# Kernel tuning notes

Hardware: AMD Instinct MI355X
Metric: run time of the kernel (lower is better)

## Reference

```python
import jax, jax.numpy as jnp
import numpy as np

N, C, T, V = 16, 64, 634, 26
K, TK = 3, 9          # spatial / temporal kernel sizes
NCLS, NAE = 60, 4     # num_classes, num_att_edge
D = C * V             # transformer d_model = 1664
NH = 4
HD = D // NH
DFF = 128
EPS = 1e-5


def _bn(x, g, b, m, v, axis=1):
    # inference-mode BatchNorm with running stats
    sh = [1] * x.ndim
    sh[axis] = -1
    return (x - m.reshape(sh)) * jax.lax.rsqrt(v.reshape(sh) + EPS) * g.reshape(sh) + b.reshape(sh)


def _ln(x, g, b):
    mu = x.mean(-1, keepdims=True)
    var = jnp.mean((x - mu) ** 2, -1, keepdims=True)
    return (x - mu) * jax.lax.rsqrt(var + EPS) * g + b


def setup_inputs() -> dict:
    ks = iter(jax.random.split(jax.random.key(0), 64))
    nrm = lambda sh, s=0.05: jax.random.normal(next(ks), sh, jnp.float32) * s
    pos = lambda sh: jax.random.uniform(next(ks), sh, jnp.float32) * 0.5 + 0.5
    return dict(
        x=jax.random.normal(next(ks), (N, C, T, V), jnp.float32),
        A=jax.random.uniform(next(ks), (K, V, V), jnp.float32) / V,
        sgc_w=nrm((3, K * C, C)), sgc_b=nrm((3, K * C)),
        M=jnp.ones((3, K, V, V), jnp.float32),
        bnA_g=pos((3, C)), bnA_b=nrm((3, C)), bnA_m=nrm((3, C)), bnA_v=pos((3, C)),
        tconv_w=nrm((3, C, C, TK)), tconv_b=nrm((3, C)),
        bnB_g=pos((3, C)), bnB_b=nrm((3, C)), bnB_m=nrm((3, C)), bnB_v=pos((3, C)),
        fc_w=nrm((NCLS, C)), fc_b=nrm((NCLS,)),
        attbn_g=pos((C,)), attbn_b=nrm((C,)), attbn_m=nrm((C,)), attbn_v=pos((C,)),
        tbn_g=pos((T,)), tbn_b=nrm((T,)), tbn_m=nrm((T,)), tbn_v=pos((T,)),
        attn_w=nrm((4, D, D), 0.02), attn_b=nrm((4, D)),
        ln1_g=pos((D,)), ln1_b=nrm((D,)),
        ff1_w=nrm((D, DFF), 0.02), ff1_b=nrm((DFF,)),
        ff2_w=nrm((DFF, D), 0.02), ff2_b=nrm((D,)),
        ln2_g=pos((D,)), ln2_b=nrm((D,)),
        attconv_w=nrm((NCLS, C)),
        nodeconv_w=nrm((1, NCLS)),
        nodebn_g=pos((1,)), nodebn_b=nrm((1,)), nodebn_m=nrm((1,)), nodebn_v=pos((1,)),
        edgeconv_w=nrm((NAE * V, NCLS)),
        edgebn_g=pos((NAE * V,)), edgebn_b=nrm((NAE * V,)), edgebn_m=nrm((NAE * V,)), edgebn_v=pos((NAE * V,)),
    )


def reference(x, A, sgc_w, sgc_b, M, bnA_g, bnA_b, bnA_m, bnA_v, tconv_w, tconv_b,
              bnB_g, bnB_b, bnB_m, bnB_v, fc_w, fc_b, attbn_g, attbn_b, attbn_m, attbn_v,
              tbn_g, tbn_b, tbn_m, tbn_v, attn_w, attn_b, ln1_g, ln1_b, ff1_w, ff1_b,
              ff2_w, ff2_b, ln2_g, ln2_b, attconv_w, nodeconv_w, nodebn_g, nodebn_b,
              nodebn_m, nodebn_v, edgeconv_w, edgebn_g, edgebn_b, edgebn_m, edgebn_v):
    h = x
    for i in range(3):  # three STGC blocks (eval-mode BN, dropout off)
        y = jnp.einsum('nctv,oc->notv', h, sgc_w[i]) + sgc_b[i][None, :, None, None]
        y = y.reshape(N, K, C, T, V)
        y = jnp.einsum('nkctv,kvw->nctw', y, A * M[i])          # spatial graph conv
        y = jax.nn.relu(_bn(y, bnA_g[i], bnA_b[i], bnA_m[i], bnA_v[i]))
        y = jax.lax.conv_general_dilated(
            y, tconv_w[i][:, :, :, None], (1, 1),
            ((TK // 2, TK // 2), (0, 0)),
            dimension_numbers=('NCHW', 'OIHW', 'NCHW')) + tconv_b[i][None, :, None, None]
        h = jax.nn.relu(_bn(y, bnB_g[i], bnB_b[i], bnB_m[i], bnB_v[i]))
    # classification head: global avg pool + 1x1 conv (== linear)
    output = h.mean((2, 3)) @ fc_w.T + fc_b                     # [N, NCLS]
    x_att = _bn(h, attbn_g, attbn_b, attbn_m, attbn_v)
    # transformer branch: computed in the original but its result is never
    # used by the returned tensors (att_mat is only printed)
    xt = h.transpose(0, 2, 1, 3).reshape(N, T, D)
    xt = _bn(xt, tbn_g, tbn_b, tbn_m, tbn_v, axis=1)            # BatchNorm1d over T channels
    q, k, v = (((xt @ attn_w[j] + attn_b[j]).reshape(N, T, NH, HD).transpose(0, 2, 1, 3)) for j in range(3))
    attn = jax.nn.softmax(jnp.einsum('nhqd,nhkd->nhqk', q, k) / HD ** 0.5, axis=-1)
    ao = jnp.einsum('nhqk,nhkd->nhqd', attn, v).transpose(0, 2, 1, 3).reshape(N, T, D)
    ao = ao @ attn_w[3] + attn_b[3]
    xb = _ln(xt + ao, ln1_g, ln1_b)
    ff = jax.nn.relu(xb @ ff1_w + ff1_b) @ ff2_w + ff2_b
    _dead = _ln(xb + ff, ln2_g, ln2_b)                          # dead: not returned
    # node attention
    x_att = jnp.einsum('nctv,oc->notv', x_att, attconv_w)       # [N, NCLS, T, V]
    x_node = jnp.einsum('nctv,oc->notv', x_att, nodeconv_w)     # [N, 1, T, V]
    x_node = _bn(x_node, nodebn_g, nodebn_b, nodebn_m, nodebn_v)
    att_node = jax.nn.sigmoid(x_node)                           # interpolate to (T,V) is identity here
    # edge attention
    x_edge = x_att.mean(2, keepdims=True)                       # avg pool over T: [N, NCLS, 1, V]
    x_edge = jnp.einsum('nctv,oc->notv', x_edge, edgeconv_w)    # [N, NAE*V, 1, V]
    x_edge = _bn(x_edge, edgebn_g, edgebn_b, edgebn_m, edgebn_v)
    att_edge = jax.nn.relu(jnp.tanh(x_edge.reshape(N, NAE, V, V)))
    return (output, att_node, att_edge)
```

## Files before the change

### kernel.cpp

```cpp
#include <hip/hip_runtime.h>
#include <hip/hip_bf16.h>
#include <math.h>

#define NN 16
#define CC 64
#define TT_ 634
#define VV 26
#define TV 16484
#define KK 3
#define OO 192
#define TKK 9
#define NCLS 60
#define NAE 4
#define EPS 1e-5f

typedef __attribute__((ext_vector_type(8))) short short8;
typedef __attribute__((ext_vector_type(4))) float f32x4;

static __device__ __forceinline__ float bf2f(unsigned int u) {
  union { unsigned int i; float f; } v; v.i = u << 16; return v.f;
}
static __device__ __forceinline__ unsigned int f2bf(float x) {
  union { float f; unsigned int i; } v; v.f = x;
  unsigned int r = v.i + 0x7fffu + ((v.i >> 16) & 1u);
  return r >> 16;
}

#define W1_ELEMS (3 * OO * CC)
#define W2_ELEMS (3 * CC * 576)
#define AM_ELEMS (3 * KK * 1024)

__global__ __launch_bounds__(256) void k_prep_all(
    const float* __restrict__ sgc_w, const float* __restrict__ tconv_w,
    const float* __restrict__ Ap, const float* __restrict__ Mp,
    unsigned short* __restrict__ W1all, unsigned short* __restrict__ W2all,
    unsigned short* __restrict__ AMall)
{
  int j = blockIdx.x * 256 + threadIdx.x;
  if (j < W1_ELEMS) { W1all[j] = (unsigned short)f2bf(sgc_w[j]); return; }
  j -= W1_ELEMS;
  if (j < W2_ELEMS) {
    const int i = j / (CC * 576), r = j % (CC * 576);
    const int c = r / 576, q = r % 576, dt = q >> 6, ci = q & 63;
    W2all[j] = (unsigned short)f2bf(
        tconv_w[(size_t)i * CC * CC * TKK + c * 576 + ci * 9 + dt]);
    return;
  }
  j -= W2_ELEMS;
  if (j < AM_ELEMS) {
    const int i = j / (KK * 1024), r = j % (KK * 1024);
    const int k = r >> 10, rr = r & 1023;
    const int w = rr >> 5, v = rr & 31;
    float val = 0.f;
    if (w < VV && v < VV)
      val = Ap[(k * VV + v) * VV + w] *
            Mp[((size_t)i * KK + k) * VV * VV + v * VV + w];
    AMall[j] = (unsigned short)f2bf(val);
  }
}

template<int F32IN>
__global__ __launch_bounds__(256) void k_fused_sgc(
    const void* __restrict__ hin,
    const unsigned short* __restrict__ W1,
    const float* __restrict__ Wb,
    const unsigned short* __restrict__ AMk,
    const float* __restrict__ bg, const float* __restrict__ bb,
    const float* __restrict__ bm, const float* __restrict__ bv,
    unsigned short* __restrict__ hout)
{
  const int NTT = 159;
  const int n = blockIdx.x / NTT, tt = blockIdx.x % NTT;
  const int t0 = tt << 2;
  const int f0 = t0 * VV;
  const int tid = threadIdx.x;
  const int wv = tid >> 6, lane = tid & 63;
  const int l15 = lane & 15, l4 = lane >> 4;

  __shared__ unsigned short sY[192 * 120];
  __shared__ float sWb[OO];
  __shared__ float sS[CC], sOff[CC];
  unsigned short* sH = sY;

  short8 amf[KK][2];
  #pragma unroll
  for (int k = 0; k < KK; ++k)
    #pragma unroll
    for (int nf = 0; nf < 2; ++nf)
      amf[k][nf] = *(const short8*)(AMk + (k << 10) + ((nf * 16 + l15) << 5)
                                    + (l4 << 3));

  const int wm0 = wv * 48;
  short8 afr[2][3];
  #pragma unroll
  for (int ks = 0; ks < 2; ++ks)
    #pragma unroll
    for (int mf = 0; mf < 3; ++mf)
      afr[ks][mf] = *(const short8*)(W1 + (size_t)(wm0 + mf * 16 + l15) * CC
                                     + (ks << 5) + (l4 << 3));

  if (tid < OO) {
    sWb[tid] = Wb[tid];
  } else if (tid >= 192) {
    const int c = tid - 192;
    const float s = bg[c] * rsqrtf(bv[c] + EPS);
    sS[c] = s;
    sOff[c] = bb[c] - bm[c] * s;
  }

  for (int it = tid; it < 14 * 64; it += 256) {
    const int ci = it & 63, fc = it >> 6;
    const int flb = fc << 3;
    const int fg = f0 + flb;
    unsigned short e[8];
    if (flb >= 104) {
      #pragma unroll
      for (int j = 0; j < 8; ++j) e[j] = 0;
    } else if (F32IN) {
      const float* hb = (const float*)hin + ((size_t)n * CC + ci) * TV;
      if (fg + 8 <= TV) {
        const float4 v0 = *(const float4*)(hb + fg);
        const float4 v1 = *(const float4*)(hb + fg + 4);
        e[0] = (unsigned short)f2bf(v0.x); e[1] = (unsigned short)f2bf(v0.y);
        e[2] = (unsigned short)f2bf(v0.z); e[3] = (unsigned short)f2bf(v0.w);
        e[4] = (unsigned short)f2bf(v1.x); e[5] = (unsigned short)f2bf(v1.y);
        e[6] = (unsigned short)f2bf(v1.z); e[7] = (unsigned short)f2bf(v1.w);
      } else {
        #pragma unroll
        for (int j = 0; j < 8; ++j)
          e[j] = (fg + j < TV) ? (unsigned short)f2bf(hb[fg + j])
                               : (unsigned short)0;
      }
    } else {
      const unsigned short* hb = (const unsigned short*)hin
                                 + ((size_t)n * CC + ci) * TV;
      if (fg + 8 <= TV) {
        const uint2 v0 = *(const uint2*)(hb + fg);
        const uint2 v1 = *(const uint2*)(hb + fg + 4);
        e[0] = (unsigned short)(v0.x & 0xffffu); e[1] = (unsigned short)(v0.x >> 16);
        e[2] = (unsigned short)(v0.y & 0xffffu); e[3] = (unsigned short)(v0.y >> 16);
        e[4] = (unsigned short)(v1.x & 0xffffu); e[5] = (unsigned short)(v1.x >> 16);
        e[6] = (unsigned short)(v1.y & 0xffffu); e[7] = (unsigned short)(v1.y >> 16);
      } else {
        #pragma unroll
        for (int j = 0; j < 8; ++j)
          e[j] = (fg + j < TV) ? hb[fg + j] : (unsigned short)0;
      }
    }
    const int cg8 = ci >> 3, cl = ci & 7;
    #pragma unroll
    for (int j = 0; j < 8; ++j)
      sH[((flb + j) << 6) + ((cg8 ^ j) << 3) + cl] = e[j];
  }
  __syncthreads();

  f32x4 acc[3][7] = {};
  #pragma unroll
  for (int ks = 0; ks < 2; ++ks) {
    short8 bfr[7];
    const int cg = (ks << 2) + l4;
    #pragma unroll
    for (int nf = 0; nf < 7; ++nf) {
      const int fl = nf * 16 + l15;
      bfr[nf] = *(const short8*)&sH[(fl << 6) + ((cg ^ (fl & 7)) << 3)];
    }
    #pragma unroll
    for (int mf = 0; mf < 3; ++mf)
      #pragma unroll
      for (int nf = 0; nf < 7; ++nf)
        acc[mf][nf] = __builtin_amdgcn_mfma_f32_16x16x32_bf16(
            afr[ks][mf], bfr[nf], acc[mf][nf], 0, 0, 0);
  }
  __syncthreads();

  #pragma unroll
  for (int mf = 0; mf < 3; ++mf)
    #pragma unroll
    for (int r = 0; r < 4; ++r) {
      const int o = wm0 + mf * 16 + (l4 << 2) + r;
      const float bias = sWb[o];
      unsigned short* yr = &sY[o * 120 + l15];
      #pragma unroll
      for (int nf = 0; nf < 7; ++nf)
        yr[nf * 16] = (unsigned short)f2bf(acc[mf][nf][r] + bias);
    }
  __syncthreads();

  const int t = t0 + wv;
  if (t < TT_) {
    f32x4 a2[4][2] = {};
    const int cuoff = wv * 13 + (l4 << 2);
    #pragma unroll
    for (int k = 0; k < KK; ++k)
      #pragma unroll
      for (int mf = 0; mf < 4; ++mf) {
        const unsigned int* rb =
            (const unsigned int*)&sY[(k * 64 + mf * 16 + l15) * 120];
        union { unsigned int u[4]; short8 s; } av;
        av.u[0] = rb[cuoff];     av.u[1] = rb[cuoff + 1];
        av.u[2] = rb[cuoff + 2]; av.u[3] = rb[cuoff + 3];
        #pragma unroll
        for (int nf = 0; nf < 2; ++nf)
          a2[mf][nf] = __builtin_amdgcn_mfma_f32_16x16x32_bf16(
              av.s, amf[k][nf], a2[mf][nf], 0, 0, 0);
      }
    #pragma unroll
    for (int mf = 0; mf < 4; ++mf)
      #pragma unroll
      for (int r = 0; r < 4; ++r) {
        const int c = mf * 16 + (l4 << 2) + r;
        const float s = sS[c], off = sOff[c];
        unsigned short* op = hout + ((size_t)n * CC + c) * TV + t * VV;
        op[l15] = (unsigned short)f2bf(fmaxf(fmaf(a2[mf][0][r], s, off), 0.f));
        if (l15 < 10)
          op[16 + l15] =
              (unsigned short)f2bf(fmaxf(fmaf(a2[mf][1][r], s, off), 0.f));
      }
  }
}

template<int F32OUT>
__global__ __launch_bounds__(256) void k_tconv_mfma(
    const unsigned short* __restrict__ xin,
    const unsigned short* __restrict__ W2,
    const float* __restrict__ wb, const float* __restrict__ bg,
    const float* __restrict__ bb, const float* __restrict__ bm,
    const float* __restrict__ bv, void* __restrict__ xout)
{
  const int NFT = (TV + 255) >> 8;
  const int n = blockIdx.x / NFT, ft = blockIdx.x % NFT;
  const int f0 = ft << 8;
  const int tid = threadIdx.x;
  const int w = tid >> 6, lane = tid & 63;
  const int l15 = lane & 15, l4 = lane >> 4;
  __shared__ unsigned short sIn[464 * 32];

  const unsigned short* xb = xin + (size_t)n * CC * TV;
  const int w64 = w << 6;
  f32x4 acc[4][4] = {};

  for (int cc = 0; cc < 2; ++cc) {
    if (cc) __syncthreads();
    for (int it = tid; it < 58 * 32; it += 256) {
      const int ci = it & 31, fc = it >> 5;
      const int flb = fc << 3;
      const int fg = f0 - 104 + flb;
      const int cig = (cc << 5) + ci;
      unsigned short e[8];
      if (fg >= 0 && fg + 8 <= TV) {
        const uint2 v0 = *(const uint2*)(xb + (size_t)cig * TV + fg);
        const uint2 v1 = *(const uint2*)(xb + (size_t)cig * TV + fg + 4);
        e[0] = (unsigned short)(v0.x & 0xffffu); e[1] = (unsigned short)(v0.x >> 16);
        e[2] = (unsigned short)(v0.y & 0xffffu); e[3] = (unsigned short)(v0.y >> 16);
        e[4] = (unsigned short)(v1.x & 0xffffu); e[5] = (unsigned short)(v1.x >> 16);
        e[6] = (unsigned short)(v1.y & 0xffffu); e[7] = (unsigned short)(v1.y >> 16);
      } else {
        #pragma unroll
        for (int j = 0; j < 8; ++j) {
          const int f = fg + j;
          e[j] = (f >= 0 && f < TV) ? xb[(size_t)cig * TV + f] : (unsigned short)0;
        }
      }
      const int cg8 = ci >> 3, cl = ci & 7;
      #pragma unroll
      for (int j = 0; j < 8; ++j) {
        const int fl = flb + j;
        sIn[(fl << 5) + ((cg8 ^ ((fl >> 1) & 3)) << 3) + cl] = e[j];
      }
    }
    __syncthreads();

    short8 wCur[4], wNxt[4];
    {
      const int koff = (cc << 5) + (l4 << 3);
      #pragma unroll
      for (int mt = 0; mt < 4; ++mt)
        wCur[mt] = *(const short8*)(W2 + (size_t)(mt * 16 + l15) * 576 + koff);
    }
    for (int dt = 0; dt < TKK; ++dt) {
      if (dt < 8) {
        const int koff = ((dt + 1) << 6) + (cc << 5) + (l4 << 3);
        #pragma unroll
        for (int mt = 0; mt < 4; ++mt)
          wNxt[mt] = *(const short8*)(W2 + (size_t)(mt * 16 + l15) * 576 + koff);
      }
      const int flb = w64 + l15 + (dt - 4) * 26 + 104;
      short8 ifr[4];
      #pragma unroll
      for (int nt = 0; nt < 4; ++nt) {
        const int fl = flb + (nt << 4);
        ifr[nt] = *(const short8*)&sIn[(fl << 5)
                                       + ((l4 ^ ((fl >> 1) & 3)) << 3)];
      }
      #pragma unroll
      for (int mt = 0; mt < 4; ++mt)
        #pragma unroll
        for (int nt = 0; nt < 4; ++nt)
          acc[mt][nt] = __builtin_amdgcn_mfma_f32_16x16x32_bf16(
              ifr[nt], wCur[mt], acc[mt][nt], 0, 0, 0);
      if (dt < 8) {
        #pragma unroll
        for (int mt = 0; mt < 4; ++mt) wCur[mt] = wNxt[mt];
      }
    }
  }

  #pragma unroll
  for (int mt = 0; mt < 4; ++mt) {
    const int c = mt * 16 + l15;
    const float sc = bg[c] * rsqrtf(bv[c] + EPS);
    const float off = fmaf(wb[c] - bm[c], sc, bb[c]);
    #pragma unroll
    for (int nt = 0; nt < 4; ++nt) {
      const int fbase = f0 + w64 + (nt << 4) + (l4 << 2);
      if (fbase < TV) {
        float v0 = fmaxf(fmaf(acc[mt][nt][0], sc, off), 0.f);
        float v1 = fmaxf(fmaf(acc[mt][nt][1], sc, off), 0.f);
        float v2 = fmaxf(fmaf(acc[mt][nt][2], sc, off), 0.f);
        float v3 = fmaxf(fmaf(acc[mt][nt][3], sc, off), 0.f);
        if (F32OUT) {
          float4 o4; o4.x = v0; o4.y = v1; o4.z = v2; o4.w = v3;
          *(float4*)((float*)xout + ((size_t)n * CC + c) * TV + fbase) = o4;
        } else {
          uint2 pk;
          pk.x = f2bf(v0) | (f2bf(v1) << 16);
          pk.y = f2bf(v2) | (f2bf(v3) << 16);
          *(uint2*)((unsigned short*)xout + ((size_t)n * CC + c) * TV + fbase) = pk;
        }
      }
    }
  }
}

__global__ __launch_bounds__(256) void k_pool(
    const float* __restrict__ h, float* __restrict__ pooled,
    float* __restrict__ hmeanv)
{
  const int tid = threadIdx.x;
  const int bid = blockIdx.x;
  const float* row = h + (size_t)bid * TV;
  __shared__ float part[9 * VV];
  if (tid < 9 * VV) {
    const int tt = tid / VV, v = tid - tt * VV;
    float s = 0.f;
    for (int t = tt; t < TT_; t += 9) s += row[t * VV + v];
    part[tid] = s;
  }
  __syncthreads();
  if (tid < VV) {
    float tot = 0.f;
    #pragma unroll
    for (int j = 0; j < 9; ++j) tot += part[j * VV + tid];
    hmeanv[(size_t)bid * VV + tid] = tot / (float)TT_;
    part[tid] = tot;
  }
  __syncthreads();
  if (tid == 0) {
    float tot = 0.f;
    for (int v = 0; v < VV; ++v) tot += part[v];
    pooled[bid] = tot / (float)TV;
  }
}

__global__ __launch_bounds__(256) void k_head_edge(
    const float* __restrict__ pooled, const float* __restrict__ hmeanv,
    const float* __restrict__ fcw, const float* __restrict__ fcb,
    const float* __restrict__ ag, const float* __restrict__ ab,
    const float* __restrict__ am, const float* __restrict__ av,
    const float* __restrict__ attw, const float* __restrict__ edgew,
    const float* __restrict__ eg, const float* __restrict__ eb,
    const float* __restrict__ em, const float* __restrict__ ev,
    float* __restrict__ dout)
{
  const int tid = threadIdx.x;
  const int n = blockIdx.x;
  __shared__ float sbnm[CC * VV];
  __shared__ float sxam[NCLS * VV];
  __shared__ float spool[CC];
  for (int i = tid; i < CC * VV; i += 256) {
    const int c = i / VV;
    const float s = ag[c] * rsqrtf(av[c] + EPS);
    const float off = ab[c] - am[c] * s;
    sbnm[i] = fmaf(hmeanv[(size_t)(n * CC) * VV + i], s, off);
  }
  if (tid < CC) spool[tid] = pooled[n * CC + tid];
  __syncthreads();
  for (int i = tid; i < NCLS * VV; i += 256) {
    const int o = i / VV, v = i - o * VV;
    float a = 0.f;
    for (int c = 0; c < CC; ++c) a = fmaf(attw[o * CC + c], sbnm[c * VV + v], a);
    sxam[i] = a;
  }
  if (tid < NCLS) {
    float a = fcb[tid];
    for (int c = 0; c < CC; ++c) a = fmaf(spool[c], fcw[tid * CC + c], a);
    dout[n * NCLS + tid] = a;
  }
  __syncthreads();
  for (int i = tid; i < NAE * VV * VV; i += 256) {
    const int j = i / VV, v = i - j * VV;
    float a = 0.f;
    for (int o = 0; o < NCLS; ++o) a = fmaf(edgew[j * NCLS + o], sxam[o * VV + v], a);
    const float s = eg[j] * rsqrtf(ev[j] + EPS);
    const float val = tanhf(fmaf(a - em[j], s, eb[j]));
    dout[NN * NCLS + (size_t)NN * TV + (size_t)n * NAE * VV * VV + i] = fmaxf(val, 0.f);
  }
}

__global__ __launch_bounds__(256) void k_node(
    const float* __restrict__ h,
    const float* __restrict__ ag, const float* __restrict__ ab,
    const float* __restrict__ am, const float* __restrict__ av,
    const float* __restrict__ attw, const float* __restrict__ nodew,
    const float* __restrict__ ng, const float* __restrict__ nb,
    const float* __restrict__ nm, const float* __restrict__ nv,
    float* __restrict__ dout)
{
  const int tid = threadIdx.x;
  __shared__ float ac[CC];
  __shared__ float tmp[CC];
  if (tid < CC) {
    float nc = 0.f;
    for (int o = 0; o < NCLS; ++o) nc = fmaf(nodew[o], attw[o * CC + tid], nc);
    const float s = ag[tid] * rsqrtf(av[tid] + EPS);
    const float off = ab[tid] - am[tid] * s;
    ac[tid] = nc * s;
    tmp[tid] = nc * off;
  }
  __syncthreads();
  if (tid == 0) {
    float b = 0.f;
    for (int c = 0; c < CC; ++c) b += tmp[c];
    tmp[0] = b;
  }
  __syncthreads();
  const float b0 = tmp[0];
  const size_t i = (size_t)blockIdx.x * 256 + tid;
  if (i < (size_t)NN * TV) {
    const int n = (int)(i / TV), f = (int)(i - (size_t)n * TV);
    const float* hb = h + (size_t)n * CC * TV + f;
    float xsum = b0;
    #pragma unroll 8
    for (int c = 0; c < CC; ++c) xsum = fmaf(hb[(size_t)c * TV], ac[c], xsum);
    const float s = ng[0] * rsqrtf(nv[0] + EPS);
    const float y = fmaf(xsum - nm[0], s, nb[0]);
    dout[NN * NCLS + i] = 1.f / (1.f + expf(-y));
  }
}

extern "C" void kernel_launch(void* const* d_in, const int* in_sizes, int n_in,
                              void* d_out, int out_size, void* d_ws, size_t ws_size,
                              hipStream_t stream) {
  const float* x        = (const float*)d_in[0];
  const float* A        = (const float*)d_in[1];
  const float* sgc_w    = (const float*)d_in[2];
  const float* sgc_b    = (const float*)d_in[3];
  const float* M        = (const float*)d_in[4];
  const float* bnA_g    = (const float*)d_in[5];
  const float* bnA_b    = (const float*)d_in[6];
  const float* bnA_m    = (const float*)d_in[7];
  const float* bnA_v    = (const float*)d_in[8];
  const float* tconv_w  = (const float*)d_in[9];
  const float* tconv_b  = (const float*)d_in[10];
  const float* bnB_g    = (const float*)d_in[11];
  const float* bnB_b    = (const float*)d_in[12];
  const float* bnB_m    = (const float*)d_in[13];
  const float* bnB_v    = (const float*)d_in[14];
  const float* fc_w     = (const float*)d_in[15];
  const float* fc_b     = (const float*)d_in[16];
  const float* attbn_g  = (const float*)d_in[17];
  const float* attbn_b  = (const float*)d_in[18];
  const float* attbn_m  = (const float*)d_in[19];
  const float* attbn_v  = (const float*)d_in[20];
  const float* attconv_w  = (const float*)d_in[35];
  const float* nodeconv_w = (const float*)d_in[36];
  const float* nodebn_g   = (const float*)d_in[37];
  const float* nodebn_b   = (const float*)d_in[38];
  const float* nodebn_m   = (const float*)d_in[39];
  const float* nodebn_v   = (const float*)d_in[40];
  const float* edgeconv_w = (const float*)d_in[41];
  const float* edgebn_g   = (const float*)d_in[42];
  const float* edgebn_b   = (const float*)d_in[43];
  const float* edgebn_m   = (const float*)d_in[44];
  const float* edgebn_v   = (const float*)d_in[45];

  float* pooled = (float*)d_ws;
  float* hmeanv = pooled + NN * CC;
  unsigned short* W1all = (unsigned short*)(hmeanv + (size_t)NN * CC * VV);
  unsigned short* W2all = W1all + W1_ELEMS;
  unsigned short* AMall = W2all + W2_ELEMS;
  unsigned short* bufA  = AMall + AM_ELEMS;
  unsigned short* bufBh = bufA + (size_t)NN * CC * TV;
  float* bufB = (float*)(bufBh + (size_t)NN * CC * TV);
  float* out = (float*)d_out;

  const int PREP_TOT = W1_ELEMS + W2_ELEMS + AM_ELEMS;
  k_prep_all<<<(PREP_TOT + 255) / 256, 256, 0, stream>>>(
      sgc_w, tconv_w, A, M, W1all, W2all, AMall);

  const int GF = NN * 159;
  const int NFC = (TV + 255) >> 8;
  for (int i = 0; i < 3; ++i) {
    const unsigned short* W1i = W1all + (size_t)i * OO * CC;
    const unsigned short* W2i = W2all + (size_t)i * CC * 576;
    const unsigned short* AMi = AMall + (size_t)i * KK * 1024;
    if (i == 0)
      k_fused_sgc<1><<<GF, 256, 0, stream>>>(
          x, W1i, sgc_b, AMi,
          bnA_g, bnA_b, bnA_m, bnA_v, bufA);
    else
      k_fused_sgc<0><<<GF, 256, 0, stream>>>(
          bufBh, W1i, sgc_b + i * OO, AMi,
          bnA_g + i * CC, bnA_b + i * CC, bnA_m + i * CC, bnA_v + i * CC,
          bufA);
    if (i < 2)
      k_tconv_mfma<0><<<NN * NFC, 256, 0, stream>>>(
          bufA, W2i, tconv_b + i * CC,
          bnB_g + i * CC, bnB_b + i * CC, bnB_m + i * CC, bnB_v + i * CC,
          (void*)bufBh);
    else
      k_tconv_mfma<1><<<NN * NFC, 256, 0, stream>>>(
          bufA, W2i, tconv_b + i * CC,
          bnB_g + i * CC, bnB_b + i * CC, bnB_m + i * CC, bnB_v + i * CC,
          (void*)bufB);
  }
  k_pool<<<NN * CC, 256, 0, stream>>>(bufB, pooled, hmeanv);
  k_head_edge<<<NN, 256, 0, stream>>>(pooled, hmeanv, fc_w, fc_b,
      attbn_g, attbn_b, attbn_m, attbn_v, attconv_w, edgeconv_w,
      edgebn_g, edgebn_b, edgebn_m, edgebn_v, out);
  k_node<<<((size_t)NN * TV + 255) / 256, 256, 0, stream>>>(
      bufB, attbn_g, attbn_b, attbn_m, attbn_v, attconv_w, nodeconv_w,
      nodebn_g, nodebn_b, nodebn_m, nodebn_v, out);
}
```

Measured before the change: 597.7 us.

## Double wavefronts per block in SGC and temporal-conv kernels, splitting MFMA tiles

Both the fused SGC kernel and the temporal-conv MFMA kernel now launch 512 threads (8 wavefronts) instead of 256. The per-wave output tile is halved: in the SGC GEMM each wave covers 64 columns instead of 112, the adjacency step splits channels across wave pairs, and in tconv each wave handles 32 columns instead of 64. The intent is more latency hiding and lower per-thread register pressure within the same tile size. The cost is that each wave now reloads its weight and adjacency fragments, padded columns are computed redundantly, and the larger block may lower how many blocks fit per compute unit.

```diff
diff --git a/kernel.cpp b/kernel.cpp
--- a/kernel.cpp
+++ b/kernel.cpp
@@ -60,7 +60,7 @@
 }
 
 template<int F32IN>
-__global__ __launch_bounds__(256) void k_fused_sgc(
+__global__ __launch_bounds__(512) void k_fused_sgc(
     const void* __restrict__ hin,
     const unsigned short* __restrict__ W1,
     const float* __restrict__ Wb,
@@ -82,33 +82,27 @@
   __shared__ float sS[CC], sOff[CC];
   unsigned short* sH = sY;
 
-  short8 amf[KK][2];
-  #pragma unroll
-  for (int k = 0; k < KK; ++k)
-    #pragma unroll
-    for (int nf = 0; nf < 2; ++nf)
-      amf[k][nf] = *(const short8*)(AMk + (k << 10) + ((nf * 16 + l15) << 5)
-                                    + (l4 << 3));
-
-  const int wm0 = wv * 48;
+  const int mq = wv >> 1;
+  const int nh = wv & 1;
+  const int m0 = mq * 48, n0 = nh << 6;
   short8 afr[2][3];
   #pragma unroll
   for (int ks = 0; ks < 2; ++ks)
     #pragma unroll
     for (int mf = 0; mf < 3; ++mf)
-      afr[ks][mf] = *(const short8*)(W1 + (size_t)(wm0 + mf * 16 + l15) * CC
+      afr[ks][mf] = *(const short8*)(W1 + (size_t)(m0 + mf * 16 + l15) * CC
                                      + (ks << 5) + (l4 << 3));
 
   if (tid < OO) {
     sWb[tid] = Wb[tid];
-  } else if (tid >= 192) {
+  } else if (tid >= 192 && tid < 256) {
     const int c = tid - 192;
     const float s = bg[c] * rsqrtf(bv[c] + EPS);
     sS[c] = s;
     sOff[c] = bb[c] - bm[c] * s;
   }
 
-  for (int it = tid; it < 14 * 64; it += 256) {
+  for (int it = tid; it < 16 * 64; it += 512) {
     const int ci = it & 63, fc = it >> 6;
     const int flb = fc << 3;
     const int fg = f0 + flb;
@@ -154,20 +148,20 @@
   }
   __syncthreads();
 
-  f32x4 acc[3][7] = {};
+  f32x4 acc[3][4] = {};
   #pragma unroll
   for (int ks = 0; ks < 2; ++ks) {
-    short8 bfr[7];
+    short8 bfr[4];
     const int cg = (ks << 2) + l4;
     #pragma unroll
-    for (int nf = 0; nf < 7; ++nf) {
-      const int fl = nf * 16 + l15;
+    for (int nf = 0; nf < 4; ++nf) {
+      const int fl = n0 + (nf << 4) + l15;
       bfr[nf] = *(const short8*)&sH[(fl << 6) + ((cg ^ (fl & 7)) << 3)];
     }
     #pragma unroll
     for (int mf = 0; mf < 3; ++mf)
       #pragma unroll
-      for (int nf = 0; nf < 7; ++nf)
+      for (int nf = 0; nf < 4; ++nf)
         acc[mf][nf] = __builtin_amdgcn_mfma_f32_16x16x32_bf16(
             afr[ks][mf], bfr[nf], acc[mf][nf], 0, 0, 0);
   }
@@ -177,25 +171,36 @@
   for (int mf = 0; mf < 3; ++mf)
     #pragma unroll
     for (int r = 0; r < 4; ++r) {
-      const int o = wm0 + mf * 16 + (l4 << 2) + r;
+      const int o = m0 + mf * 16 + (l4 << 2) + r;
       const float bias = sWb[o];
-      unsigned short* yr = &sY[o * 120 + l15];
-      #pragma unroll
-      for (int nf = 0; nf < 7; ++nf)
-        yr[nf * 16] = (unsigned short)f2bf(acc[mf][nf][r] + bias);
-    }
-  __syncthreads();
-
-  const int t = t0 + wv;
+      #pragma unroll
+      for (int nf = 0; nf < 4; ++nf) {
+        const int col = n0 + (nf << 4) + l15;
+        if (col < 112)
+          sY[o * 120 + col] = (unsigned short)f2bf(acc[mf][nf][r] + bias);
+      }
+    }
+  __syncthreads();
+
+  const int tl = wv >> 1;
+  const int ch = wv & 1;
+  const int t = t0 + tl;
   if (t < TT_) {
-    f32x4 a2[4][2] = {};
-    const int cuoff = wv * 13 + (l4 << 2);
+    short8 amf[KK][2];
     #pragma unroll
     for (int k = 0; k < KK; ++k)
       #pragma unroll
-      for (int mf = 0; mf < 4; ++mf) {
+      for (int nf = 0; nf < 2; ++nf)
+        amf[k][nf] = *(const short8*)(AMk + (k << 10) + ((nf * 16 + l15) << 5)
+                                      + (l4 << 3));
+    f32x4 a2[2][2] = {};
+    const int cuoff = tl * 13 + (l4 << 2);
+    #pragma unroll
+    for (int k = 0; k < KK; ++k)
+      #pragma unroll
+      for (int mf = 0; mf < 2; ++mf) {
         const unsigned int* rb =
-            (const unsigned int*)&sY[(k * 64 + mf * 16 + l15) * 120];
+            (const unsigned int*)&sY[(k * 64 + (ch << 5) + mf * 16 + l15) * 120];
         union { unsigned int u[4]; short8 s; } av;
         av.u[0] = rb[cuoff];     av.u[1] = rb[cuoff + 1];
         av.u[2] = rb[cuoff + 2]; av.u[3] = rb[cuoff + 3];
@@ -205,10 +210,10 @@
               av.s, amf[k][nf], a2[mf][nf], 0, 0, 0);
       }
     #pragma unroll
-    for (int mf = 0; mf < 4; ++mf)
+    for (int mf = 0; mf < 2; ++mf)
       #pragma unroll
       for (int r = 0; r < 4; ++r) {
-        const int c = mf * 16 + (l4 << 2) + r;
+        const int c = (ch << 5) + mf * 16 + (l4 << 2) + r;
         const float s = sS[c], off = sOff[c];
         unsigned short* op = hout + ((size_t)n * CC + c) * TV + t * VV;
         op[l15] = (unsigned short)f2bf(fmaxf(fmaf(a2[mf][0][r], s, off), 0.f));
@@ -220,7 +225,7 @@
 }
 
 template<int F32OUT>
-__global__ __launch_bounds__(256) void k_tconv_mfma(
+__global__ __launch_bounds__(512) void k_tconv_mfma(
     const unsigned short* __restrict__ xin,
     const unsigned short* __restrict__ W2,
     const float* __restrict__ wb, const float* __restrict__ bg,
@@ -236,12 +241,12 @@
   __shared__ unsigned short sIn[464 * 32];
 
   const unsigned short* xb = xin + (size_t)n * CC * TV;
-  const int w64 = w << 6;
-  f32x4 acc[4][4] = {};
+  const int wf0 = w << 5;
+  f32x4 acc[4][2] = {};
 
   for (int cc = 0; cc < 2; ++cc) {
     if (cc) __syncthreads();
-    for (int it = tid; it < 58 * 32; it += 256) {
+    for (int it = tid; it < 58 * 32; it += 512) {
       const int ci = it & 31, fc = it >> 5;
       const int flb = fc << 3;
       const int fg = f0 - 104 + flb;
@@ -284,10 +289,10 @@
         for (int mt = 0; mt < 4; ++mt)
           wNxt[mt] = *(const short8*)(W2 + (size_t)(mt * 16 + l15) * 576 + koff);
       }
-      const int flb = w64 + l15 + (dt - 4) * 26 + 104;
-      short8 ifr[4];
-      #pragma unroll
-      for (int nt = 0; nt < 4; ++nt) {
+      const int flb = wf0 + l15 + (dt - 4) * 26 + 104;
+      short8 ifr[2];
+      #pragma unroll
+      for (int nt = 0; nt < 2; ++nt) {
         const int fl = flb + (nt << 4);
         ifr[nt] = *(const short8*)&sIn[(fl << 5)
                                        + ((l4 ^ ((fl >> 1) & 3)) << 3)];
@@ -295,7 +300,7 @@
       #pragma unroll
       for (int mt = 0; mt < 4; ++mt)
         #pragma unroll
-        for (int nt = 0; nt < 4; ++nt)
+        for (int nt = 0; nt < 2; ++nt)
           acc[mt][nt] = __builtin_amdgcn_mfma_f32_16x16x32_bf16(
               ifr[nt], wCur[mt], acc[mt][nt], 0, 0, 0);
       if (dt < 8) {
@@ -311,8 +316,8 @@
     const float sc = bg[c] * rsqrtf(bv[c] + EPS);
     const float off = fmaf(wb[c] - bm[c], sc, bb[c]);
     #pragma unroll
-    for (int nt = 0; nt < 4; ++nt) {
-      const int fbase = f0 + w64 + (nt << 4) + (l4 << 2);
+    for (int nt = 0; nt < 2; ++nt) {
+      const int fbase = f0 + wf0 + (nt << 4) + (l4 << 2);
       if (fbase < TV) {
         float v0 = fmaxf(fmaf(acc[mt][nt][0], sc, off), 0.f);
         float v1 = fmaxf(fmaf(acc[mt][nt][1], sc, off), 0.f);
@@ -505,21 +510,21 @@
     const unsigned short* W2i = W2all + (size_t)i * CC * 576;
     const unsigned short* AMi = AMall + (size_t)i * KK * 1024;
     if (i == 0)
-      k_fused_sgc<1><<<GF, 256, 0, stream>>>(
+      k_fused_sgc<1><<<GF, 512, 0, stream>>>(
           x, W1i, sgc_b, AMi,
           bnA_g, bnA_b, bnA_m, bnA_v, bufA);
     else
-      k_fused_sgc<0><<<GF, 256, 0, stream>>>(
+      k_fused_sgc<0><<<GF, 512, 0, stream>>>(
           bufBh, W1i, sgc_b + i * OO, AMi,
           bnA_g + i * CC, bnA_b + i * CC, bnA_m + i * CC, bnA_v + i * CC,
           bufA);
     if (i < 2)
-      k_tconv_mfma<0><<<NN * NFC, 256, 0, stream>>>(
+      k_tconv_mfma<0><<<NN * NFC, 512, 0, stream>>>(
           bufA, W2i, tconv_b + i * CC,
           bnB_g + i * CC, bnB_b + i * CC, bnB_m + i * CC, bnB_v + i * CC,
           (void*)bufBh);
     else
-      k_tconv_mfma<1><<<NN * NFC, 256, 0, stream>>>(
+      k_tconv_mfma<1><<<NN * NFC, 512, 0, stream>>>(
           bufA, W2i, tconv_b + i * CC,
           bnB_g + i * CC, bnB_b + i * CC, bnB_m + i * CC, bnB_v + i * CC,
           (void*)bufB);
```

Measured after the change: 667.3 us. 1.12x slower.
